# Optimization experiments

Measured on AMD Instinct MI355X. Metric: run time of the kernel, lower is better.

Reference implementation:

```python
import jax, jax.numpy as jnp
import numpy as np

B = 128        # graphs
NPG = 64       # nodes per graph (num_node)
N = B * NPG    # total nodes = 8192
IN = 16        # in_channels
D = 128        # d_model
OUT = 64       # out_channels
CAT = IN * NPG + NPG * NPG  # 5120
EPS = 1e-5


def _lin_init(k, fi, fo):
    s = 1.0 / np.sqrt(fi)
    kw, kb = jax.random.split(k)
    W = jax.random.uniform(kw, (fi, fo), jnp.float32, -s, s)
    b = jax.random.uniform(kb, (fo,), jnp.float32, -s, s)
    return W, b


def setup_inputs() -> dict:
    key = jax.random.key(0)
    ks = jax.random.split(key, 10)
    x = jax.random.normal(ks[0], (N, IN), jnp.float32)
    # complete graph (all i->j pairs, incl. self loops) per graph, offset per graph
    ii = np.repeat(np.arange(NPG), NPG)
    jj = np.tile(np.arange(NPG), NPG)
    off = (np.arange(B) * NPG)[:, None]
    row = (ii[None, :] + off).reshape(-1)
    col = (jj[None, :] + off).reshape(-1)
    edge_index = jnp.asarray(np.stack([row, col]), jnp.int32)  # [2, E]
    E = edge_index.shape[1]
    edge_weight = jax.random.uniform(ks[1], (E,), jnp.float32)
    batch = jnp.repeat(jnp.arange(B, dtype=jnp.int32), NPG)
    W1, b1 = _lin_init(ks[2], IN, D)
    W2, b2 = _lin_init(ks[3], D, D)
    Wm0, bm0 = _lin_init(ks[4], D + CAT, D)
    Wm1, bm1 = _lin_init(ks[5], D, D)
    Wm2, bm2 = _lin_init(ks[6], D, D)
    Wout, bout = _lin_init(ks[7], D, OUT)
    ones = jnp.ones((D,), jnp.float32)
    zeros = jnp.zeros((D,), jnp.float32)
    return dict(x=x, edge_index=edge_index, edge_weight=edge_weight, batch=batch,
                W1=W1, b1=b1, W2=W2, b2=b2,
                Wm0=Wm0, bm0=bm0, g0=ones, be0=zeros,
                Wm1=Wm1, bm1=bm1, g1=ones, be1=zeros,
                Wm2=Wm2, bm2=bm2, g2=ones, be2=zeros,
                Wout=Wout, bout=bout)


def _gcn_conv(h_in, row, col, ew, W, b):
    # PyG GCNConv: linear first, then D^-1/2 (A) D^-1/2 aggregation (self loops already present)
    h = h_in @ W                                             # [N, F]
    deg = jax.ops.segment_sum(ew, col, num_segments=N)       # in-degree by edge weight
    dinv = jnp.where(deg > 0, jax.lax.rsqrt(deg), 0.0)
    norm = dinv[row] * ew * dinv[col]                        # [E]
    out = jax.ops.segment_sum(norm[:, None] * h[row], col, num_segments=N)
    return out + b


def _bn(h, g, b):
    # BatchNorm1d, training-mode math (biased variance), eps=1e-5
    m = jnp.mean(h, axis=0)
    v = jnp.var(h, axis=0)
    return g * (h - m) * jax.lax.rsqrt(v + EPS) + b


def reference(x, edge_index, edge_weight, batch,
              W1, b1, W2, b2,
              Wm0, bm0, g0, be0,
              Wm1, bm1, g1, be1,
              Wm2, bm2, g2, be2,
              Wout, bout):
    row, col = edge_index[0], edge_index[1]
    h = _gcn_conv(x, row, col, edge_weight, W1, b1)
    h = jax.nn.relu(h)
    h = _gcn_conv(h, row, col, edge_weight, W2, b2)
    # global_mean_pool
    sums = jax.ops.segment_sum(h, batch, num_segments=B)
    cnt = jax.ops.segment_sum(jnp.ones((N,), h.dtype), batch, num_segments=B)
    pooled = sums / cnt[:, None]
    pooled = jax.nn.relu(pooled)
    feat = jnp.concatenate([pooled, x.reshape(B, -1), edge_weight.reshape(B, -1)], axis=1)
    feat = jax.nn.relu(feat)
    h = _bn(jax.nn.relu(feat @ Wm0 + bm0), g0, be0)
    h = _bn(jax.nn.relu(h @ Wm1 + bm1), g1, be1)
    h = _bn(jax.nn.relu(h @ Wm2 + bm2), g2, be2)
    return h @ Wout + bout
```

## Files before the change

kernel.cpp:

```cpp
#include <hip/hip_runtime.h>

#define NPG 64
#define IN 16
#define DM 128
#define NOUT 64
#define EPG 4096
#define BN_EPS 1e-5f

__device__ __forceinline__ void stg(float* p, float v) {
    __hip_atomic_store(p, v, __ATOMIC_RELAXED, __HIP_MEMORY_SCOPE_AGENT);
}
__device__ __forceinline__ float lda(const float* p) {
    return __hip_atomic_load(p, __ATOMIC_RELAXED, __HIP_MEMORY_SCOPE_AGENT);
}

__device__ __forceinline__ void gbar(unsigned* bu, unsigned e, int bid, int t,
                                     bool wait) {
    __syncthreads();
    if (t == 0) {
        unsigned* sub   = bu + e * 160 + (bid & 7) * 16;
        unsigned* root  = bu + e * 160 + 128;
        unsigned* flags = bu + 1024;
        if (atomicAdd(sub, 1u) == 31u)
            if (atomicAdd(root, 1u) == 7u)
                for (int i = 0; i < 256; i++)
                    __hip_atomic_store(&flags[i * 16], e,
                                       __ATOMIC_RELAXED, __HIP_MEMORY_SCOPE_AGENT);
        if (wait)
            while (__hip_atomic_load(&flags[bid * 16],
                                     __ATOMIC_RELAXED, __HIP_MEMORY_SCOPE_AGENT) < e)
                __builtin_amdgcn_s_sleep(1);
    }
    __syncthreads();
}

__device__ void mlp_phase(float* u,
    const float* __restrict__ vin, const float* __restrict__ statsin,
    const float* __restrict__ gbn, const float* __restrict__ bbn,
    const float* __restrict__ W, const float* __restrict__ bias,
    float* __restrict__ vout, float* __restrict__ statsout)
{
    float* scale_s = u;
    float* shift_s = u + 128;
    float* wcol    = u + 256;
    float* pc      = u + 384;
    float* h_s     = u + 640;
    const int b = blockIdx.x, t = threadIdx.x;
    const int f = b & 127, gh = b >> 7;
    if (t < 128) {
        float s1 = lda(&statsin[t * 2]), s2 = lda(&statsin[t * 2 + 1]);
        float m = s1 * (1.f / 128.f);
        float var = s2 * (1.f / 128.f) - m * m;
        float sc = gbn[t] * rsqrtf(var + BN_EPS);
        scale_s[t] = sc;
        shift_s[t] = bbn[t] - m * sc;
        wcol[t] = W[t * 128 + f];
    }
    __syncthreads();
    const float* vbase = vin + (size_t)gh * 64 * 128;
    {
        const int k = t & 127;
        const float sck = scale_s[k], shk = shift_s[k];
        #pragma unroll
        for (int it = 0; it < 32; ++it) {
            int idx = it * 256 + t;
            int gl = idx >> 7;
            h_s[gl * 129 + k] = lda(&vbase[idx]) * sck + shk;
        }
    }
    __syncthreads();
    {
        const int gl = t & 63, kh = t >> 6;
        float acc = 0.f;
        #pragma unroll 8
        for (int k = kh * 32; k < kh * 32 + 32; ++k)
            acc += h_s[gl * 129 + k] * wcol[k];
        pc[gl * 4 + kh] = acc;
    }
    __syncthreads();
    if (t < 64) {
        float v = fmaxf(pc[t * 4] + pc[t * 4 + 1] + pc[t * 4 + 2] + pc[t * 4 + 3]
                        + bias[f], 0.f);
        stg(&vout[(size_t)(gh * 64 + t) * 128 + f], v);
        float s1 = v, s2 = v * v;
        #pragma unroll
        for (int off = 32; off > 0; off >>= 1) {
            s1 += __shfl_down(s1, off, 64);
            s2 += __shfl_down(s2, off, 64);
        }
        if (t == 0) {
            atomicAdd(&statsout[f * 2], s1);
            atomicAdd(&statsout[f * 2 + 1], s2);
        }
    }
}

__global__ __launch_bounds__(256) void k_fused(
    const float* __restrict__ x, const float* __restrict__ ew,
    const float* __restrict__ W1, const float* __restrict__ b1,
    const float* __restrict__ W2, const float* __restrict__ b2,
    const float* __restrict__ Wm0, const float* __restrict__ bm0,
    const float* __restrict__ gbn0, const float* __restrict__ bbn0,
    const float* __restrict__ Wm1, const float* __restrict__ bm1,
    const float* __restrict__ gbn1, const float* __restrict__ bbn1,
    const float* __restrict__ Wm2, const float* __restrict__ bm2,
    const float* __restrict__ gbn2, const float* __restrict__ bbn2,
    const float* __restrict__ Wo, const float* __restrict__ bo,
    float* __restrict__ ws, float* __restrict__ out)
{
    __shared__ __align__(16) float u[16128];
    unsigned* bu = (unsigned*)ws;
    float* stats = ws + 5120;
    float* part  = ws + 6144;
    float* ppart = part + 64 * 8192;
    float* v0 = ppart + 16384;
    float* v1 = v0 + 16384;
    float* v2 = v1 + 16384;
    const int bid = blockIdx.x, t = threadIdx.x;

    if (bid < 128) {
        float* ew_s     = u;
        float* x_s      = u + 4096;
        float* W1_s     = u + 5120;
        float* P_s      = u + 7168;
        float* b1_s     = u + 15360;
        float* dinv_s   = u + 15488;
        float* t_s      = u + 15552;
        float* zp       = u + 4096;
        float* z_full   = u + 15616;
        float* pooled_s = u + 15744;
        float* pp2      = u + 15872;
        const int g = bid;
        {
            const float4* ew4 = (const float4*)(ew + g * EPG);
            float4* ews4 = (float4*)ew_s;
            #pragma unroll
            for (int i = 0; i < 4; i++) ews4[t + 256 * i] = ew4[t + 256 * i];
            const int xi = t & 63, k4 = (t >> 6) * 4;
            float4 xv = *(const float4*)(x + g * NPG * IN + xi * IN + k4);
            x_s[(k4 + 0) * 64 + xi] = xv.x;
            x_s[(k4 + 1) * 64 + xi] = xv.y;
            x_s[(k4 + 2) * 64 + xi] = xv.z;
            x_s[(k4 + 3) * 64 + xi] = xv.w;
            ((float4*)W1_s)[t]       = ((const float4*)W1)[t];
            ((float4*)W1_s)[t + 256] = ((const float4*)W1)[t + 256];
            if (t < 128) b1_s[t] = b1[t];
        }
        __syncthreads();

        if (t < NPG) {
            float s = 0.f;
            #pragma unroll 8
            for (int i = 0; i < NPG; i++) s += ew_s[i * NPG + t];
            dinv_s[t] = (s > 0.f) ? rsqrtf(s) : 0.f;
        }
        __syncthreads();

        {
            const int j = t & 63, q = t >> 6;
            const float dj = dinv_s[j];
            for (int i = q * 16; i < q * 16 + 16; i++) {
                float vv = ew_s[i * NPG + j] * dj;
                #pragma unroll
                for (int off = 32; off > 0; off >>= 1) vv += __shfl_down(vv, off, 64);
                if (j == 0) t_s[i] = dinv_s[i] * vv * (1.f / 64.f);
            }
        }

        {
            const int it = t & 15, ft = t >> 4;
            const int i0 = it * 4, f0 = ft * 8;
            float accp[4][8];
            #pragma unroll
            for (int a = 0; a < 4; a++)
                #pragma unroll
                for (int c = 0; c < 8; c++) accp[a][c] = 0.f;
            #pragma unroll
            for (int k = 0; k < IN; k++) {
                const float4 a4  = *(const float4*)(x_s + k * 64 + i0);
                const float4 b0v = *(const float4*)(W1_s + k * DM + f0);
                const float4 b1v = *(const float4*)(W1_s + k * DM + f0 + 4);
                const float av[4] = {a4.x, a4.y, a4.z, a4.w};
                const float bv[8] = {b0v.x, b0v.y, b0v.z, b0v.w, b1v.x, b1v.y, b1v.z, b1v.w};
                #pragma unroll
                for (int a = 0; a < 4; a++)
                    #pragma unroll
                    for (int c = 0; c < 8; c++) accp[a][c] += av[a] * bv[c];
            }
            #pragma unroll
            for (int a = 0; a < 4; a++) {
                const float di = dinv_s[i0 + a];
                float4* o = (float4*)(P_s + (i0 + a) * DM + f0);
                o[0] = make_float4(di * accp[a][0], di * accp[a][1],
                                   di * accp[a][2], di * accp[a][3]);
                o[1] = make_float4(di * accp[a][4], di * accp[a][5],
                                   di * accp[a][6], di * accp[a][7]);
            }
        }
        __syncthreads();

        {
            const int jt = t & 15, ft = t >> 4;
            const int j0 = jt * 4, f0 = ft * 8;
            float acc[4][8];
            #pragma unroll
            for (int a = 0; a < 4; a++)
                #pragma unroll
                for (int c = 0; c < 8; c++) acc[a][c] = 0.f;
            #pragma unroll 4
            for (int k = 0; k < 64; k++) {
                const float4 a4  = *(const float4*)(ew_s + k * 64 + j0);
                const float4 b0v = *(const float4*)(P_s + k * DM + f0);
                const float4 b1v = *(const float4*)(P_s + k * DM + f0 + 4);
                const float av[4] = {a4.x, a4.y, a4.z, a4.w};
                const float bv[8] = {b0v.x, b0v.y, b0v.z, b0v.w, b1v.x, b1v.y, b1v.z, b1v.w};
                #pragma unroll
                for (int a = 0; a < 4; a++)
                    #pragma unroll
                    for (int c = 0; c < 8; c++) acc[a][c] += av[a] * bv[c];
            }
            float zpart[8];
            #pragma unroll
            for (int c = 0; c < 8; c++) zpart[c] = 0.f;
            #pragma unroll
            for (int a = 0; a < 4; a++) {
                const float dj = dinv_s[j0 + a], tj = t_s[j0 + a];
                #pragma unroll
                for (int c = 0; c < 8; c++) {
                    float h = fmaxf(dj * acc[a][c] + b1_s[f0 + c], 0.f);
                    zpart[c] += tj * h;
                }
            }
            float4* zo = (float4*)(zp + jt * 132 + f0);
            zo[0] = make_float4(zpart[0], zpart[1], zpart[2], zpart[3]);
            zo[1] = make_float4(zpart[4], zpart[5], zpart[6], zpart[7]);
        }
        __syncthreads();

        if (t < 128) {
            float s = 0.f;
            #pragma unroll
            for (int jt = 0; jt < 16; jt++) s += zp[jt * 132 + t];
            z_full[t] = s;
        }
        __syncthreads();

        {
            const int c = t & 127, kh = t >> 7;
            float acc = 0.f;
            #pragma unroll 8
            for (int k = kh * 64; k < kh * 64 + 64; k++)
                acc += z_full[k] * W2[k * DM + c];
            pp2[kh * 128 + c] = acc;
        }
        __syncthreads();
        if (t < 128) pooled_s[t] = fmaxf(pp2[t] + pp2[128 + t] + b2[t], 0.f);
        __syncthreads();

        {
            const int f = t & 127, kh = t >> 7;
            float acc = 0.f;
            #pragma unroll 8
            for (int k = kh * 64; k < kh * 64 + 64; k++)
                acc += pooled_s[k] * Wm0[k * DM + f];
            pp2[kh * 128 + f] = acc;
        }
        __syncthreads();
        if (t < 128) stg(&ppart[g * DM + t], pp2[t] + pp2[128 + t]);
    } else if (bid < 192) {
        const int c = bid - 128;
        const int kc = c >> 1, fh = c & 1;
        float* a_s = u;
        float* b_s = u + 10560;

        const int gthr = t & 31, fthr = t >> 5;
        const int g0 = gthr * 4, f0 = fthr * 8;
        float acc[4][8];
        #pragma unroll
        for (int i = 0; i < 4; i++)
            #pragma unroll
            for (int jx = 0; jx < 8; jx++) acc[i][jx] = 0.f;

        for (int pass = 0; pass < 2; pass++) {
            const int K0 = kc * 160 + pass * 80;
            float4 va[8], vb2[2], vc[5];
            #pragma unroll
            for (int it = 0; it < 8; it++) {
                int idx = it * 256 + t;
                int gg = idx >> 4, k4 = (idx & 15) << 2;
                int K = K0 + k4;
                const float* src = (K < 1024) ? (x + gg * 1024 + K)
                                              : (ew + gg * 4096 + (K - 1024));
                va[it] = *(const float4*)src;
            }
            #pragma unroll
            for (int it = 0; it < 2; it++) {
                int idx = it * 256 + t;
                int gg = idx >> 2, k4 = 64 + ((idx & 3) << 2);
                int K = K0 + k4;
                const float* src = (K < 1024) ? (x + gg * 1024 + K)
                                              : (ew + gg * 4096 + (K - 1024));
                vb2[it] = *(const float4*)src;
            }
            #pragma unroll
            for (int it = 0; it < 5; it++) {
                int idx = it * 256 + t;
                int k = idx >> 4, fl4 = (idx & 15) << 2;
                vc[it] = *(const float4*)(Wm0 + (size_t)(128 + K0 + k) * 128
                                          + fh * 64 + fl4);
            }
            #pragma unroll
            for (int it = 0; it < 8; it++) {
                int idx = it * 256 + t;
                int gg = idx >> 4, k4 = (idx & 15) << 2;
                a_s[(k4 + 0) * 132 + gg] = fmaxf(va[it].x, 0.f);
                a_s[(k4 + 1) * 132 + gg] = fmaxf(va[it].y, 0.f);
                a_s[(k4 + 2) * 132 + gg] = fmaxf(va[it].z, 0.f);
                a_s[(k4 + 3) * 132 + gg] = fmaxf(va[it].w, 0.f);
            }
            #pragma unroll
            for (int it = 0; it < 2; it++) {
                int idx = it * 256 + t;
                int gg = idx >> 2, k4 = 64 + ((idx & 3) << 2);
                a_s[(k4 + 0) * 132 + gg] = fmaxf(vb2[it].x, 0.f);
                a_s[(k4 + 1) * 132 + gg] = fmaxf(vb2[it].y, 0.f);
                a_s[(k4 + 2) * 132 + gg] = fmaxf(vb2[it].z, 0.f);
                a_s[(k4 + 3) * 132 + gg] = fmaxf(vb2[it].w, 0.f);
            }
            #pragma unroll
            for (int it = 0; it < 5; it++) {
                int idx = it * 256 + t;
                int k = idx >> 4, fl4 = (idx & 15) << 2;
                *(float4*)(b_s + k * 64 + fl4) = vc[it];
            }
            __syncthreads();

            #pragma unroll 4
            for (int k = 0; k < 80; k++) {
                const float4 a4  = *(const float4*)(a_s + k * 132 + g0);
                const float4 c0v = *(const float4*)(b_s + k * 64 + f0);
                const float4 c1v = *(const float4*)(b_s + k * 64 + f0 + 4);
                const float av[4] = {a4.x, a4.y, a4.z, a4.w};
                const float bv[8] = {c0v.x, c0v.y, c0v.z, c0v.w, c1v.x, c1v.y, c1v.z, c1v.w};
                #pragma unroll
                for (int i = 0; i < 4; i++)
                    #pragma unroll
                    for (int jx = 0; jx < 8; jx++) acc[i][jx] += av[i] * bv[jx];
            }
            __syncthreads();
        }

        float* pp = part + (size_t)c * 8192;
        #pragma unroll
        for (int i = 0; i < 4; i++) {
            const int base = (g0 + i) * 64 + f0;
            #pragma unroll
            for (int jx = 0; jx < 8; jx++) stg(&pp[base + jx], acc[i][jx]);
        }
    }
    gbar(bu, 1u, bid, t, true);

    {
        float* r1  = u;
        float* sv  = u + 1024;
        float* sv2 = u + 1088;
        const int fgrp = bid & 7, gt = bid >> 3;
        const int f4 = t & 3, gl = (t >> 2) & 3, ch = t >> 4;
        const int g = gt * 4 + gl;
        const int fbase = fgrp * 16 + f4 * 4;
        const int fh = fbase >> 6, fl = fbase & 63;
        float r0v = 0.f, r1v = 0.f, r2v = 0.f, r3v = 0.f;
        #pragma unroll
        for (int q = 0; q < 2; q++) {
            const int kc = ch + q * 16;
            const float* p = part + (size_t)(kc * 2 + fh) * 8192 + g * 64 + fl;
            r0v += lda(&p[0]); r1v += lda(&p[1]);
            r2v += lda(&p[2]); r3v += lda(&p[3]);
        }
        float* r = r1 + ch * 64 + gl * 16 + f4 * 4;
        r[0] = r0v; r[1] = r1v; r[2] = r2v; r[3] = r3v;
        __syncthreads();

        if (t < 64) {
            const int fsub = t & 15, gl2 = t >> 4;
            const int f = fgrp * 16 + fsub, gg = gt * 4 + gl2;
            float s = bm0[f] + lda(&ppart[gg * DM + f]);
            #pragma unroll
            for (int c2 = 0; c2 < 16; c2++) s += r1[c2 * 64 + gl2 * 16 + fsub];
            s = fmaxf(s, 0.f);
            stg(&v0[gg * DM + f], s);
            sv[t] = s; sv2[t] = s * s;
        }
        __syncthreads();
        if (t < 16) {
            float s1 = sv[t] + sv[t + 16] + sv[t + 32] + sv[t + 48];
            float s2 = sv2[t] + sv2[t + 16] + sv2[t + 32] + sv2[t + 48];
            atomicAdd(&stats[(fgrp * 16 + t) * 2], s1);
            atomicAdd(&stats[(fgrp * 16 + t) * 2 + 1], s2);
        }
    }
    gbar(bu, 2u, bid, t, true);

    mlp_phase(u, v0, stats,       gbn0, bbn0, Wm1, bm1, v1, stats + 256);
    gbar(bu, 3u, bid, t, true);
    mlp_phase(u, v1, stats + 256, gbn1, bbn1, Wm2, bm2, v2, stats + 512);
    gbar(bu, 4u, bid, t, bid < 128);
    if (bid >= 128) return;

    {
        float* Wo_s = u;
        float* vrow = u + 8192;
        float* sc   = u + 8320;
        float* sh   = u + 8448;
        float* pc   = u + 8576;
        const float* st2 = stats + 512;
        const int g = bid;
        if (t < 128) {
            float s1 = lda(&st2[t * 2]), s2 = lda(&st2[t * 2 + 1]);
            float m = s1 * (1.f / 128.f);
            float var = s2 * (1.f / 128.f) - m * m;
            float scv = gbn2[t] * rsqrtf(var + BN_EPS);
            sc[t] = scv;
            sh[t] = bbn2[t] - m * scv;
        }
        {
            const float4* wo4 = (const float4*)Wo;
            float4* wos4 = (float4*)Wo_s;
            #pragma unroll
            for (int it = 0; it < 8; it++) wos4[it * 256 + t] = wo4[it * 256 + t];
        }
        __syncthreads();
        if (t < 128) vrow[t] = lda(&v2[(size_t)g * 128 + t]) * sc[t] + sh[t];
        __syncthreads();
        {
            const int o = t & 63, kh = t >> 6;
            float acc = 0.f;
            #pragma unroll 8
            for (int k = kh * 32; k < kh * 32 + 32; k++)
                acc += vrow[k] * Wo_s[k * 64 + o];
            pc[kh * 64 + o] = acc;
        }
        __syncthreads();
        if (t < 64)
            out[g * NOUT + t] = pc[t] + pc[64 + t] + pc[128 + t] + pc[192 + t] + bo[t];
    }
}

extern "C" void kernel_launch(void* const* d_in, const int* in_sizes, int n_in,
                              void* d_out, int out_size, void* d_ws, size_t ws_size,
                              hipStream_t stream)
{
    const float* x   = (const float*)d_in[0];
    const float* ew  = (const float*)d_in[2];
    const float* W1  = (const float*)d_in[4];
    const float* b1  = (const float*)d_in[5];
    const float* W2  = (const float*)d_in[6];
    const float* b2  = (const float*)d_in[7];
    const float* Wm0 = (const float*)d_in[8];
    const float* bm0 = (const float*)d_in[9];
    const float* g0  = (const float*)d_in[10];
    const float* be0 = (const float*)d_in[11];
    const float* Wm1 = (const float*)d_in[12];
    const float* bm1 = (const float*)d_in[13];
    const float* g1  = (const float*)d_in[14];
    const float* be1 = (const float*)d_in[15];
    const float* Wm2 = (const float*)d_in[16];
    const float* bm2 = (const float*)d_in[17];
    const float* g2  = (const float*)d_in[18];
    const float* be2 = (const float*)d_in[19];
    const float* Wo  = (const float*)d_in[20];
    const float* bo  = (const float*)d_in[21];

    float* ws = (float*)d_ws;
    hipMemsetAsync(d_ws, 0, 24576, stream);
    k_fused<<<256, 256, 0, stream>>>(x, ew, W1, b1, W2, b2,
                                     Wm0, bm0, g0, be0,
                                     Wm1, bm1, g1, be1,
                                     Wm2, bm2, g2, be2,
                                     Wo, bo, ws, (float*)d_out);
}
```

Baseline: 151.1 us.

## Remove grid barrier by recomputing BatchNorm stats redundantly per block

Drops one grid-wide barrier and the atomic stats buffers. Every block now re-reads the full 128x128 activation slab and computes the BatchNorm mean and variance locally, and the first MLP layer fuses in the reduction of the Wm0 partial sums. The big Wm0 GEMM is re-split into 4 K-chunks over 32x32 output tiles, double-buffered in LDS. An acquire fence is added after the barrier wait so plain loads can replace atomic loads. The cost is redundant global reads of the slab in every block and a longer K loop per GEMM block.

```diff
diff --git a/kernel.cpp b/kernel.cpp
--- a/kernel.cpp
+++ b/kernel.cpp
@@ -9,9 +9,6 @@
 
 __device__ __forceinline__ void stg(float* p, float v) {
     __hip_atomic_store(p, v, __ATOMIC_RELAXED, __HIP_MEMORY_SCOPE_AGENT);
-}
-__device__ __forceinline__ float lda(const float* p) {
-    return __hip_atomic_load(p, __ATOMIC_RELAXED, __HIP_MEMORY_SCOPE_AGENT);
 }
 
 __device__ __forceinline__ void gbar(unsigned* bu, unsigned e, int bid, int t,
@@ -26,47 +23,77 @@
                 for (int i = 0; i < 256; i++)
                     __hip_atomic_store(&flags[i * 16], e,
                                        __ATOMIC_RELAXED, __HIP_MEMORY_SCOPE_AGENT);
-        if (wait)
+        if (wait) {
             while (__hip_atomic_load(&flags[bid * 16],
                                      __ATOMIC_RELAXED, __HIP_MEMORY_SCOPE_AGENT) < e)
                 __builtin_amdgcn_s_sleep(1);
+            __builtin_amdgcn_fence(__ATOMIC_ACQUIRE, "agent");
+        }
     }
     __syncthreads();
 }
 
-__device__ void mlp_phase(float* u,
-    const float* __restrict__ vin, const float* __restrict__ statsin,
+__device__ void mlp_slab(float* u, int bid, int t,
+    const float* __restrict__ part, const float* __restrict__ ppart,
+    const float* __restrict__ bm0,
     const float* __restrict__ gbn, const float* __restrict__ bbn,
     const float* __restrict__ W, const float* __restrict__ bias,
-    float* __restrict__ vout, float* __restrict__ statsout)
+    float* __restrict__ vout)
 {
-    float* scale_s = u;
-    float* shift_s = u + 128;
-    float* wcol    = u + 256;
-    float* pc      = u + 384;
-    float* h_s     = u + 640;
-    const int b = blockIdx.x, t = threadIdx.x;
-    const int f = b & 127, gh = b >> 7;
+    float* h_s  = u;
+    float* sp1  = u + 8256;
+    float* sp2  = u + 9280;
+    float* sc   = u + 10304;
+    float* sh   = u + 10432;
+    float* wcol = u + 10560;
+    float* pc   = u + 10688;
+    const int f = bid & 127, gh = bid >> 7;
+    if (t < 128) wcol[t] = W[t * 128 + f];
+    const int f4 = (t & 31) * 4, tg = t >> 5;
+    const float4 b4 = *(const float4*)(bm0 + f4);
+    const bool own = (tg >> 2) == gh;
+    float s1a[4] = {0.f, 0.f, 0.f, 0.f}, s2a[4] = {0.f, 0.f, 0.f, 0.f};
+    #pragma unroll 4
+    for (int i = 0; i < 16; i++) {
+        const int g = tg * 16 + i;
+        float4 v = *(const float4*)(ppart + g * 128 + f4);
+        v.x += b4.x; v.y += b4.y; v.z += b4.z; v.w += b4.w;
+        #pragma unroll
+        for (int kc = 0; kc < 4; kc++) {
+            float4 p = *(const float4*)(part + kc * 16384 + g * 128 + f4);
+            v.x += p.x; v.y += p.y; v.z += p.z; v.w += p.w;
+        }
+        v.x = fmaxf(v.x, 0.f); v.y = fmaxf(v.y, 0.f);
+        v.z = fmaxf(v.z, 0.f); v.w = fmaxf(v.w, 0.f);
+        s1a[0] += v.x; s1a[1] += v.y; s1a[2] += v.z; s1a[3] += v.w;
+        s2a[0] += v.x * v.x; s2a[1] += v.y * v.y;
+        s2a[2] += v.z * v.z; s2a[3] += v.w * v.w;
+        if (own) {
+            const int r = g & 63;
+            h_s[r * 129 + f4 + 0] = v.x; h_s[r * 129 + f4 + 1] = v.y;
+            h_s[r * 129 + f4 + 2] = v.z; h_s[r * 129 + f4 + 3] = v.w;
+        }
+    }
+    #pragma unroll
+    for (int j = 0; j < 4; j++) {
+        sp1[tg * 128 + f4 + j] = s1a[j];
+        sp2[tg * 128 + f4 + j] = s2a[j];
+    }
+    __syncthreads();
     if (t < 128) {
-        float s1 = lda(&statsin[t * 2]), s2 = lda(&statsin[t * 2 + 1]);
-        float m = s1 * (1.f / 128.f);
-        float var = s2 * (1.f / 128.f) - m * m;
-        float sc = gbn[t] * rsqrtf(var + BN_EPS);
-        scale_s[t] = sc;
-        shift_s[t] = bbn[t] - m * sc;
-        wcol[t] = W[t * 128 + f];
-    }
-    __syncthreads();
-    const float* vbase = vin + (size_t)gh * 64 * 128;
-    {
-        const int k = t & 127;
-        const float sck = scale_s[k], shk = shift_s[k];
+        float S1 = 0.f, S2 = 0.f;
         #pragma unroll
-        for (int it = 0; it < 32; ++it) {
-            int idx = it * 256 + t;
-            int gl = idx >> 7;
-            h_s[gl * 129 + k] = lda(&vbase[idx]) * sck + shk;
-        }
+        for (int q = 0; q < 8; q++) { S1 += sp1[q * 128 + t]; S2 += sp2[q * 128 + t]; }
+        float m = S1 * (1.f / 128.f);
+        float var = S2 * (1.f / 128.f) - m * m;
+        float s = gbn[t] * rsqrtf(var + BN_EPS);
+        sc[t] = s; sh[t] = bbn[t] - m * s;
+    }
+    __syncthreads();
+    #pragma unroll
+    for (int e = t; e < 8192; e += 256) {
+        int g = e >> 7, k = e & 127;
+        h_s[g * 129 + k] = h_s[g * 129 + k] * sc[k] + sh[k];
     }
     __syncthreads();
     {
@@ -82,16 +109,75 @@
         float v = fmaxf(pc[t * 4] + pc[t * 4 + 1] + pc[t * 4 + 2] + pc[t * 4 + 3]
                         + bias[f], 0.f);
         stg(&vout[(size_t)(gh * 64 + t) * 128 + f], v);
-        float s1 = v, s2 = v * v;
+    }
+}
+
+__device__ void mlp_v(float* u, int bid, int t,
+    const float* __restrict__ vin,
+    const float* __restrict__ gbn, const float* __restrict__ bbn,
+    const float* __restrict__ W, const float* __restrict__ bias,
+    float* __restrict__ vout)
+{
+    float* h_s  = u;
+    float* sp1  = u + 8256;
+    float* sp2  = u + 9280;
+    float* sc   = u + 10304;
+    float* sh   = u + 10432;
+    float* wcol = u + 10560;
+    float* pc   = u + 10688;
+    const int f = bid & 127, gh = bid >> 7;
+    if (t < 128) wcol[t] = W[t * 128 + f];
+    const int f4 = (t & 31) * 4, tg = t >> 5;
+    const bool own = (tg >> 2) == gh;
+    float s1a[4] = {0.f, 0.f, 0.f, 0.f}, s2a[4] = {0.f, 0.f, 0.f, 0.f};
+    #pragma unroll 4
+    for (int i = 0; i < 16; i++) {
+        const int g = tg * 16 + i;
+        float4 v = *(const float4*)(vin + (size_t)g * 128 + f4);
+        s1a[0] += v.x; s1a[1] += v.y; s1a[2] += v.z; s1a[3] += v.w;
+        s2a[0] += v.x * v.x; s2a[1] += v.y * v.y;
+        s2a[2] += v.z * v.z; s2a[3] += v.w * v.w;
+        if (own) {
+            const int r = g & 63;
+            h_s[r * 129 + f4 + 0] = v.x; h_s[r * 129 + f4 + 1] = v.y;
+            h_s[r * 129 + f4 + 2] = v.z; h_s[r * 129 + f4 + 3] = v.w;
+        }
+    }
+    #pragma unroll
+    for (int j = 0; j < 4; j++) {
+        sp1[tg * 128 + f4 + j] = s1a[j];
+        sp2[tg * 128 + f4 + j] = s2a[j];
+    }
+    __syncthreads();
+    if (t < 128) {
+        float S1 = 0.f, S2 = 0.f;
         #pragma unroll
-        for (int off = 32; off > 0; off >>= 1) {
-            s1 += __shfl_down(s1, off, 64);
-            s2 += __shfl_down(s2, off, 64);
-        }
-        if (t == 0) {
-            atomicAdd(&statsout[f * 2], s1);
-            atomicAdd(&statsout[f * 2 + 1], s2);
-        }
+        for (int q = 0; q < 8; q++) { S1 += sp1[q * 128 + t]; S2 += sp2[q * 128 + t]; }
+        float m = S1 * (1.f / 128.f);
+        float var = S2 * (1.f / 128.f) - m * m;
+        float s = gbn[t] * rsqrtf(var + BN_EPS);
+        sc[t] = s; sh[t] = bbn[t] - m * s;
+    }
+    __syncthreads();
+    #pragma unroll
+    for (int e = t; e < 8192; e += 256) {
+        int g = e >> 7, k = e & 127;
+        h_s[g * 129 + k] = h_s[g * 129 + k] * sc[k] + sh[k];
+    }
+    __syncthreads();
+    {
+        const int gl = t & 63, kh = t >> 6;
+        float acc = 0.f;
+        #pragma unroll 8
+        for (int k = kh * 32; k < kh * 32 + 32; ++k)
+            acc += h_s[gl * 129 + k] * wcol[k];
+        pc[gl * 4 + kh] = acc;
+    }
+    __syncthreads();
+    if (t < 64) {
+        float v = fmaxf(pc[t * 4] + pc[t * 4 + 1] + pc[t * 4 + 2] + pc[t * 4 + 3]
+                        + bias[f], 0.f);
+        stg(&vout[(size_t)(gh * 64 + t) * 128 + f], v);
     }
 }
 
@@ -110,11 +196,9 @@
 {
     __shared__ __align__(16) float u[16128];
     unsigned* bu = (unsigned*)ws;
-    float* stats = ws + 5120;
-    float* part  = ws + 6144;
-    float* ppart = part + 64 * 8192;
-    float* v0 = ppart + 16384;
-    float* v1 = v0 + 16384;
+    float* part  = ws + 5120;
+    float* ppart = part + 65536;
+    float* v1 = ppart + 16384;
     float* v2 = v1 + 16384;
     const int bid = blockIdx.x, t = threadIdx.x;
 
@@ -269,168 +353,122 @@
         if (t < 128) stg(&ppart[g * DM + t], pp2[t] + pp2[128 + t]);
     } else if (bid < 192) {
         const int c = bid - 128;
-        const int kc = c >> 1, fh = c & 1;
+        const int gt = c & 3, fq = (c >> 2) & 3, kc = c >> 4;
+        const int g0 = gt * 32, f0 = fq * 32, K0 = kc * 1280;
         float* a_s = u;
-        float* b_s = u + 10560;
-
-        const int gthr = t & 31, fthr = t >> 5;
-        const int g0 = gthr * 4, f0 = fthr * 8;
-        float acc[4][8];
-        #pragma unroll
-        for (int i = 0; i < 4; i++)
-            #pragma unroll
-            for (int jx = 0; jx < 8; jx++) acc[i][jx] = 0.f;
-
-        for (int pass = 0; pass < 2; pass++) {
-            const int K0 = kc * 160 + pass * 80;
-            float4 va[8], vb2[2], vc[5];
-            #pragma unroll
-            for (int it = 0; it < 8; it++) {
-                int idx = it * 256 + t;
-                int gg = idx >> 4, k4 = (idx & 15) << 2;
-                int K = K0 + k4;
-                const float* src = (K < 1024) ? (x + gg * 1024 + K)
-                                              : (ew + gg * 4096 + (K - 1024));
-                va[it] = *(const float4*)src;
-            }
+        float* b_s = u + 4864;
+        const int gq = t & 15, ft = t >> 4;
+        float a00 = 0.f, a01 = 0.f, a10 = 0.f, a11 = 0.f;
+        float4 ra[2], rb[2];
+
+        auto LOAD = [&](int ci) {
             #pragma unroll
             for (int it = 0; it < 2; it++) {
                 int idx = it * 256 + t;
-                int gg = idx >> 2, k4 = 64 + ((idx & 3) << 2);
-                int K = K0 + k4;
-                const float* src = (K < 1024) ? (x + gg * 1024 + K)
-                                              : (ew + gg * 4096 + (K - 1024));
-                vb2[it] = *(const float4*)src;
-            }
-            #pragma unroll
-            for (int it = 0; it < 5; it++) {
-                int idx = it * 256 + t;
-                int k = idx >> 4, fl4 = (idx & 15) << 2;
-                vc[it] = *(const float4*)(Wm0 + (size_t)(128 + K0 + k) * 128
-                                          + fh * 64 + fl4);
-            }
-            #pragma unroll
-            for (int it = 0; it < 8; it++) {
-                int idx = it * 256 + t;
-                int gg = idx >> 4, k4 = (idx & 15) << 2;
-                a_s[(k4 + 0) * 132 + gg] = fmaxf(va[it].x, 0.f);
-                a_s[(k4 + 1) * 132 + gg] = fmaxf(va[it].y, 0.f);
-                a_s[(k4 + 2) * 132 + gg] = fmaxf(va[it].z, 0.f);
-                a_s[(k4 + 3) * 132 + gg] = fmaxf(va[it].w, 0.f);
-            }
+                int gg = idx >> 4, k4 = (idx & 15) * 4;
+                int K = K0 + ci * 64 + k4;
+                const float* src = (K < 1024) ? (x + (size_t)(g0 + gg) * 1024 + K)
+                                              : (ew + (size_t)(g0 + gg) * 4096 + (K - 1024));
+                ra[it] = *(const float4*)src;
+                int kB = idx >> 3, fB = (idx & 7) * 4;
+                rb[it] = *(const float4*)(Wm0 + (size_t)(128 + K0 + ci * 64 + kB) * 128
+                                          + f0 + fB);
+            }
+        };
+        auto STORE = [&](int buf) {
+            float* ab = a_s + buf * 2432;
+            float* bb = b_s + buf * 2432;
             #pragma unroll
             for (int it = 0; it < 2; it++) {
                 int idx = it * 256 + t;
-                int gg = idx >> 2, k4 = 64 + ((idx & 3) << 2);
-                a_s[(k4 + 0) * 132 + gg] = fmaxf(vb2[it].x, 0.f);
-                a_s[(k4 + 1) * 132 + gg] = fmaxf(vb2[it].y, 0.f);
-                a_s[(k4 + 2) * 132 + gg] = fmaxf(vb2[it].z, 0.f);
-                a_s[(k4 + 3) * 132 + gg] = fmaxf(vb2[it].w, 0.f);
-            }
-            #pragma unroll
-            for (int it = 0; it < 5; it++) {
-                int idx = it * 256 + t;
-                int k = idx >> 4, fl4 = (idx & 15) << 2;
-                *(float4*)(b_s + k * 64 + fl4) = vc[it];
-            }
+                int gg = idx >> 4, k4 = (idx & 15) * 4;
+                ab[(k4 + 0) * 38 + gg] = fmaxf(ra[it].x, 0.f);
+                ab[(k4 + 1) * 38 + gg] = fmaxf(ra[it].y, 0.f);
+                ab[(k4 + 2) * 38 + gg] = fmaxf(ra[it].z, 0.f);
+                ab[(k4 + 3) * 38 + gg] = fmaxf(ra[it].w, 0.f);
+                int kB = idx >> 3, fB = (idx & 7) * 4;
+                bb[kB * 38 + fB + 0] = rb[it].x;
+                bb[kB * 38 + fB + 1] = rb[it].y;
+                bb[kB * 38 + fB + 2] = rb[it].z;
+                bb[kB * 38 + fB + 3] = rb[it].w;
+            }
+        };
+        auto COMP = [&](int buf) {
+            const float* ab = a_s + buf * 2432 + gq * 2;
+            const float* bb = b_s + buf * 2432 + ft * 2;
+            #pragma unroll 8
+            for (int k = 0; k < 64; k++) {
+                float x0 = ab[k * 38], x1 = ab[k * 38 + 1];
+                float y0 = bb[k * 38], y1 = bb[k * 38 + 1];
+                a00 += x0 * y0; a01 += x0 * y1;
+                a10 += x1 * y0; a11 += x1 * y1;
+            }
+        };
+
+        LOAD(0); STORE(0);
+        __syncthreads();
+        for (int ci = 0; ci < 20; ci++) {
+            if (ci < 19) LOAD(ci + 1);
+            COMP(ci & 1);
+            if (ci < 19) STORE((ci + 1) & 1);
             __syncthreads();
-
-            #pragma unroll 4
-            for (int k = 0; k < 80; k++) {
-                const float4 a4  = *(const float4*)(a_s + k * 132 + g0);
-                const float4 c0v = *(const float4*)(b_s + k * 64 + f0);
-                const float4 c1v = *(const float4*)(b_s + k * 64 + f0 + 4);
-                const float av[4] = {a4.x, a4.y, a4.z, a4.w};
-                const float bv[8] = {c0v.x, c0v.y, c0v.z, c0v.w, c1v.x, c1v.y, c1v.z, c1v.w};
-                #pragma unroll
-                for (int i = 0; i < 4; i++)
-                    #pragma unroll
-                    for (int jx = 0; jx < 8; jx++) acc[i][jx] += av[i] * bv[jx];
-            }
-            __syncthreads();
-        }
-
-        float* pp = part + (size_t)c * 8192;
-        #pragma unroll
-        for (int i = 0; i < 4; i++) {
-            const int base = (g0 + i) * 64 + f0;
-            #pragma unroll
-            for (int jx = 0; jx < 8; jx++) stg(&pp[base + jx], acc[i][jx]);
-        }
+        }
+        const int gb = g0 + gq * 2, fb = f0 + ft * 2;
+        stg(&part[kc * 16384 + (gb + 0) * 128 + fb + 0], a00);
+        stg(&part[kc * 16384 + (gb + 0) * 128 + fb + 1], a01);
+        stg(&part[kc * 16384 + (gb + 1) * 128 + fb + 0], a10);
+        stg(&part[kc * 16384 + (gb + 1) * 128 + fb + 1], a11);
     }
     gbar(bu, 1u, bid, t, true);
 
-    {
-        float* r1  = u;
-        float* sv  = u + 1024;
-        float* sv2 = u + 1088;
-        const int fgrp = bid & 7, gt = bid >> 3;
-        const int f4 = t & 3, gl = (t >> 2) & 3, ch = t >> 4;
-        const int g = gt * 4 + gl;
-        const int fbase = fgrp * 16 + f4 * 4;
-        const int fh = fbase >> 6, fl = fbase & 63;
-        float r0v = 0.f, r1v = 0.f, r2v = 0.f, r3v = 0.f;
-        #pragma unroll
-        for (int q = 0; q < 2; q++) {
-            const int kc = ch + q * 16;
-            const float* p = part + (size_t)(kc * 2 + fh) * 8192 + g * 64 + fl;
-            r0v += lda(&p[0]); r1v += lda(&p[1]);
-            r2v += lda(&p[2]); r3v += lda(&p[3]);
-        }
-        float* r = r1 + ch * 64 + gl * 16 + f4 * 4;
-        r[0] = r0v; r[1] = r1v; r[2] = r2v; r[3] = r3v;
-        __syncthreads();
-
-        if (t < 64) {
-            const int fsub = t & 15, gl2 = t >> 4;
-            const int f = fgrp * 16 + fsub, gg = gt * 4 + gl2;
-            float s = bm0[f] + lda(&ppart[gg * DM + f]);
-            #pragma unroll
-            for (int c2 = 0; c2 < 16; c2++) s += r1[c2 * 64 + gl2 * 16 + fsub];
-            s = fmaxf(s, 0.f);
-            stg(&v0[gg * DM + f], s);
-            sv[t] = s; sv2[t] = s * s;
-        }
-        __syncthreads();
-        if (t < 16) {
-            float s1 = sv[t] + sv[t + 16] + sv[t + 32] + sv[t + 48];
-            float s2 = sv2[t] + sv2[t + 16] + sv2[t + 32] + sv2[t + 48];
-            atomicAdd(&stats[(fgrp * 16 + t) * 2], s1);
-            atomicAdd(&stats[(fgrp * 16 + t) * 2 + 1], s2);
-        }
-    }
+    mlp_slab(u, bid, t, part, ppart, bm0, gbn0, bbn0, Wm1, bm1, v1);
     gbar(bu, 2u, bid, t, true);
-
-    mlp_phase(u, v0, stats,       gbn0, bbn0, Wm1, bm1, v1, stats + 256);
-    gbar(bu, 3u, bid, t, true);
-    mlp_phase(u, v1, stats + 256, gbn1, bbn1, Wm2, bm2, v2, stats + 512);
-    gbar(bu, 4u, bid, t, bid < 128);
+    mlp_v(u, bid, t, v1, gbn1, bbn1, Wm2, bm2, v2);
+    gbar(bu, 3u, bid, t, bid < 128);
     if (bid >= 128) return;
 
     {
         float* Wo_s = u;
-        float* vrow = u + 8192;
-        float* sc   = u + 8320;
-        float* sh   = u + 8448;
-        float* pc   = u + 8576;
-        const float* st2 = stats + 512;
+        float* sp1  = u + 8192;
+        float* sp2  = u + 9216;
+        float* sc   = u + 10240;
+        float* sh   = u + 10368;
+        float* vrow = u + 10496;
+        float* pc   = u + 10624;
         const int g = bid;
-        if (t < 128) {
-            float s1 = lda(&st2[t * 2]), s2 = lda(&st2[t * 2 + 1]);
-            float m = s1 * (1.f / 128.f);
-            float var = s2 * (1.f / 128.f) - m * m;
-            float scv = gbn2[t] * rsqrtf(var + BN_EPS);
-            sc[t] = scv;
-            sh[t] = bbn2[t] - m * scv;
-        }
         {
             const float4* wo4 = (const float4*)Wo;
             float4* wos4 = (float4*)Wo_s;
             #pragma unroll
             for (int it = 0; it < 8; it++) wos4[it * 256 + t] = wo4[it * 256 + t];
         }
-        __syncthreads();
-        if (t < 128) vrow[t] = lda(&v2[(size_t)g * 128 + t]) * sc[t] + sh[t];
+        const int f4 = (t & 31) * 4, tg = t >> 5;
+        float s1a[4] = {0.f, 0.f, 0.f, 0.f}, s2a[4] = {0.f, 0.f, 0.f, 0.f};
+        #pragma unroll 4
+        for (int i = 0; i < 16; i++) {
+            const int g2 = tg * 16 + i;
+            float4 v = *(const float4*)(v2 + (size_t)g2 * 128 + f4);
+            s1a[0] += v.x; s1a[1] += v.y; s1a[2] += v.z; s1a[3] += v.w;
+            s2a[0] += v.x * v.x; s2a[1] += v.y * v.y;
+            s2a[2] += v.z * v.z; s2a[3] += v.w * v.w;
+        }
+        #pragma unroll
+        for (int j = 0; j < 4; j++) {
+            sp1[tg * 128 + f4 + j] = s1a[j];
+            sp2[tg * 128 + f4 + j] = s2a[j];
+        }
+        __syncthreads();
+        if (t < 128) {
+            float S1 = 0.f, S2 = 0.f;
+            #pragma unroll
+            for (int q = 0; q < 8; q++) { S1 += sp1[q * 128 + t]; S2 += sp2[q * 128 + t]; }
+            float m = S1 * (1.f / 128.f);
+            float var = S2 * (1.f / 128.f) - m * m;
+            float s = gbn2[t] * rsqrtf(var + BN_EPS);
+            sc[t] = s; sh[t] = bbn2[t] - m * s;
+        }
+        __syncthreads();
+        if (t < 128) vrow[t] = v2[(size_t)g * 128 + t] * sc[t] + sh[t];
         __syncthreads();
         {
             const int o = t & 63, kh = t >> 6;
@@ -472,7 +510,7 @@
     const float* bo  = (const float*)d_in[21];
 
     float* ws = (float*)d_ws;
-    hipMemsetAsync(d_ws, 0, 24576, stream);
+    hipMemsetAsync(d_ws, 0, 20480, stream);
     k_fused<<<256, 256, 0, stream>>>(x, ew, W1, b1, W2, b2,
                                      Wm0, bm0, g0, be0,
                                      Wm1, bm1, g1, be1,
```

Measured after the change: 154.5 us. 1.02x slower.
